# Optimization experiments

Measured on AMD Instinct MI355X. Metric: run time of the kernel, lower is better.

The kernel has to match this reference:

```python
import jax, jax.numpy as jnp
import numpy as np
from jax import lax

# Config (matches init_kwargs): TrajGRU per HKO-7 reference impl (Shi et al.)
B, T, Cin, H, W = 8, 12, 1, 128, 128
F_, L = 64, 5            # out_channels (hidden filters), num trajectories
h_, w_ = H // 2, W // 2  # post-downsample spatial size


def _conv(x, w, b, stride=1, pad=0):
    y = lax.conv_general_dilated(x, w, (stride, stride), [(pad, pad), (pad, pad)],
                                 dimension_numbers=('NCHW', 'OIHW', 'NCHW'))
    return y + b[None, :, None, None]


def _leaky(x):
    return jnp.where(x >= 0, x, 0.2 * x)  # LeakyReLU(0.2)


def _warp_multi(img, flows):
    # img: (B,C,h,w); flows: (B,L,2,h,w) pixel displacements.
    # Bilinear grid_sample with zero padding; the HKO normalization
    # (2*v/(W-1)-1) followed by align_corners=True denormalization is the
    # identity, so we sample directly at grid + flow in pixel space.
    Bb, C, Hh, Ww = img.shape
    x = jnp.arange(Ww, dtype=img.dtype)[None, None, None, :] + flows[:, :, 0]  # (B,L,h,w)
    y = jnp.arange(Hh, dtype=img.dtype)[None, None, :, None] + flows[:, :, 1]
    x0 = jnp.floor(x); y0 = jnp.floor(y)
    x1 = x0 + 1.0;     y1 = y0 + 1.0
    imgl = img.transpose(0, 2, 3, 1)  # (B,h,w,C)
    bidx = jnp.arange(Bb)[:, None, None, None]

    def gather(xi, yi):
        valid = (xi >= 0) & (xi <= Ww - 1) & (yi >= 0) & (yi <= Hh - 1)
        xic = jnp.clip(xi, 0, Ww - 1).astype(jnp.int32)
        yic = jnp.clip(yi, 0, Hh - 1).astype(jnp.int32)
        return imgl[bidx, yic, xic] * valid[..., None].astype(img.dtype)  # (B,L,h,w,C)

    wa = ((x1 - x) * (y1 - y))[..., None]
    wb = ((x1 - x) * (y - y0))[..., None]
    wc = ((x - x0) * (y1 - y))[..., None]
    wd = ((x - x0) * (y - y0))[..., None]
    out = wa * gather(x0, y0) + wb * gather(x0, y1) + wc * gather(x1, y0) + wd * gather(x1, y1)
    # concat L warped copies along channels: (B,L,h,w,C) -> (B, L*C, h, w)
    return out.transpose(0, 1, 4, 2, 3).reshape(Bb, L * C, Hh, Ww)


def setup_inputs() -> dict:
    key = jax.random.key(0)
    ks = jax.random.split(key, 13)
    def rn(k, shape, s=0.05):
        return jax.random.normal(k, shape, dtype=jnp.float32) * s
    return {
        'x': jax.random.normal(ks[0], (B, T, Cin, H, W), dtype=jnp.float32),
        'W_down': rn(ks[1], (F_ * T, Cin * T, 4, 4)),
        'b_down': rn(ks[2], (F_ * T,)),
        'W_i2h': rn(ks[3], (3 * F_, F_, 3, 3)),
        'b_i2h': rn(ks[4], (3 * F_,)),
        'W_i2f': rn(ks[5], (32, F_, 5, 5)),
        'b_i2f': rn(ks[6], (32,)),
        'W_h2f': rn(ks[7], (32, F_, 5, 5)),
        'b_h2f': rn(ks[8], (32,)),
        'W_flow': rn(ks[9], (2 * L, 32, 5, 5), 0.02),
        'b_flow': rn(ks[10], (2 * L,), 0.02),
        'W_ret': rn(ks[11], (3 * F_, L * F_, 1, 1)),
        'b_ret': rn(ks[12], (3 * F_,)),
    }


def reference(x, W_down, b_down, W_i2h, b_i2h, W_i2f, b_i2f, W_h2f, b_h2f,
              W_flow, b_flow, W_ret, b_ret):
    Bb = x.shape[0]
    # downsample conv (k=4,s=2,p=1) + LeakyReLU(0.2) on time-stacked channels
    xd = _leaky(_conv(x.reshape(Bb, T * Cin, H, W), W_down, b_down, stride=2, pad=1))
    seq = xd.reshape(Bb, T, F_, h_, w_).transpose(1, 0, 2, 3, 4)  # (T,B,F,h,w)

    # input-dependent convs are batched across all timesteps up front
    flat = seq.reshape(T * Bb, F_, h_, w_)
    i2h_all = _conv(flat, W_i2h, b_i2h, pad=1).reshape(T, Bb, 3 * F_, h_, w_)
    i2f_all = _conv(flat, W_i2f, b_i2f, pad=2).reshape(T, Bb, 32, h_, w_)

    def step(hprev, inp):
        i2h_t, i2f_t = inp
        # flow generator: leaky(i2f(x_t) + h2f(h)) -> flows conv -> L 2-ch flows
        f1 = _leaky(i2f_t + _conv(hprev, W_h2f, b_h2f, pad=2))
        flows = _conv(f1, W_flow, b_flow, pad=2).reshape(Bb, L, 2, h_, w_)
        warped = _warp_multi(hprev, -flows)          # (B, L*F, h, w)
        h2h = _conv(warped, W_ret, b_ret)            # 1x1 projection -> (B, 3F, h, w)
        ir, iu, im = jnp.split(i2h_t, 3, axis=1)
        hr, hu, hm = jnp.split(h2h, 3, axis=1)
        r = jax.nn.sigmoid(ir + hr)
        u = jax.nn.sigmoid(iu + hu)
        m = _leaky(im + r * hm)
        hnew = u * hprev + (1.0 - u) * m
        return hnew, hnew

    h0 = jnp.zeros((Bb, F_, h_, w_), x.dtype)
    _, outs = lax.scan(step, h0, (i2h_all, i2f_all))  # (T,B,F,h,w)
    return outs.transpose(1, 0, 2, 3, 4)              # (B,T,F,h,w)
```

## Files before the change

### kernel.cpp

```cpp
#include <hip/hip_runtime.h>
#include <cstdint>

typedef long long ll;
typedef __bf16 bf16x8 __attribute__((ext_vector_type(8)));
typedef float f32x4 __attribute__((ext_vector_type(4)));
typedef unsigned int u32x4 __attribute__((ext_vector_type(4)));

#define NB 8
#define NT 12
#define NF 64
#define HWSZ 4096
#define I2H_T ((ll)NB * 4096 * 192)
#define I2F_T ((ll)NB * 4096 * 32)

struct alignas(8)  bh4 { __bf16 h[4]; };
struct alignas(16) bh8 { __bf16 h[8]; };

static __device__ inline f32x4 mfma16(bf16x8 a, bf16x8 b, f32x4 c) {
  return __builtin_amdgcn_mfma_f32_16x16x32_bf16(a, b, c, 0, 0, 0);
}
static __device__ inline bf16x8 ld8(const __bf16* p) {
  u32x4 u = *(const u32x4*)p;
  return __builtin_bit_cast(bf16x8, u);
}
static __device__ inline void st4(__bf16* p, float a0, float a1, float a2, float a3) {
  bh4 t; t.h[0] = (__bf16)a0; t.h[1] = (__bf16)a1; t.h[2] = (__bf16)a2; t.h[3] = (__bf16)a3;
  *(bh4*)p = t;
}
static __device__ inline float lky(float a) { return a >= 0.f ? a : 0.2f * a; }

static __device__ inline int swz_bid() {
  int bid = blockIdx.x;
  return ((gridDim.x & 7) == 0) ? (bid & 7) * (gridDim.x >> 3) + (bid >> 3) : bid;
}

static __device__ inline void step_decode(int& b, int& y, int& xh) {
  int bid = blockIdx.x;
  int oct = bid & 7, s = bid >> 3;
  b = s >> 4;
  int r = s & 15;
  y = oct * 8 + (r >> 1);
  xh = r & 1;
}

template<int W, int HALO>
static __device__ void stage8(__bf16* dst, const __bf16* grow) {
  int tid = threadIdx.x;
  u32x4 zz = {0u, 0u, 0u, 0u};
  #pragma unroll
  for (int it = 0; it < 2; ++it) {
    int i = tid + it * 256;
    int xr = i >> 3, g = i & 7, xi = xr + HALO;
    u32x4 v = zz;
    if (grow) v = *(const u32x4*)(grow + xr * 64 + g * 8);
    *(u32x4*)(dst + (g * W + xi) * 8) = v;
  }
  if (tid < 16 * HALO) {
    int h = tid >> 3, g = tid & 7;
    int xi = (h < HALO) ? h : 64 + h;
    *(u32x4*)(dst + (g * W + xi) * 8) = zz;
  }
}

__global__ __launch_bounds__(256) void k_prep(
    const float* __restrict__ Wd, const float* __restrict__ Wc,
    const float* __restrict__ Wi, const float* __restrict__ Wh,
    const float* __restrict__ Wfl, const float* __restrict__ Wret,
    __bf16* __restrict__ Adown, __bf16* __restrict__ Ai2h,
    __bf16* __restrict__ Afi, __bf16* __restrict__ Afh,
    __bf16* __restrict__ Afl, __bf16* __restrict__ Aret) {
  int n = blockIdx.x * 256 + threadIdx.x;
  if (n < 147456) {
    Adown[n] = (__bf16)Wd[n];
  } else if (n < 258048) {
    int i = n - 147456;
    int tap = i / 12288, o = (i % 12288) / 64, c = i % 64;
    Ai2h[i] = (__bf16)Wc[(o * 64 + c) * 9 + tap];
  } else if (n < 309248) {
    int i = n - 258048;
    int tap = i / 2048, o = (i % 2048) / 64, c = i % 64;
    Afi[i] = (__bf16)Wi[(o * 64 + c) * 25 + tap];
  } else if (n < 360448) {
    int i = n - 309248;
    int tap = i / 2048, o = (i % 2048) / 64, c = i % 64;
    Afh[i] = (__bf16)Wh[(o * 64 + c) * 25 + tap];
  } else if (n < 373248) {
    int i = n - 360448;
    int tap = i / 512, o = (i % 512) / 32, c = i % 32;
    Afl[i] = (__bf16)(o < 10 ? Wfl[(o * 32 + c) * 25 + tap] : 0.f);
  } else if (n < 434688) {
    Aret[n - 373248] = (__bf16)Wret[n - 373248];
  }
}

__global__ __launch_bounds__(256) void k_down(
    const float* __restrict__ x, const __bf16* __restrict__ Adown,
    const float* __restrict__ bd, __bf16* __restrict__ seq) {
  __shared__ __bf16 smd[6240];
  int bi = swz_bid();
  int zQ = bi & 3, y = (bi >> 2) & 63, b = bi >> 8;
  int tid = threadIdx.x;
  for (int i = tid; i < 6240; i += 256) {
    int ic = i / 520, rem = i % 520, ky = rem / 130, xi = rem % 130;
    int ix = xi - 1, iy = 2 * y - 1 + ky;
    float v = (ix >= 0 && ix < 128 && iy >= 0 && iy < 128)
                  ? x[(((ll)(b * 12 + ic) * 128 + iy) << 7) + ix] : 0.f;
    smd[i] = (__bf16)v;
  }
  __syncthreads();
  int wv = __builtin_amdgcn_readfirstlane(tid >> 6);
  int lane = tid & 63, q = lane >> 4, lr = lane & 15;
  int px = wv * 16 + lr;
  f32x4 zv = {0.f, 0.f, 0.f, 0.f};
  f32x4 acc[12];
  #pragma unroll
  for (int mt = 0; mt < 12; ++mt) acc[mt] = zv;

  for (int ks = 0; ks < 6; ++ks) {
    int k0 = ks * 32 + q * 8;
    int ic = k0 >> 4, ky0 = (k0 >> 2) & 3;
    const __bf16* rp = smd + (ic * 4 + ky0) * 130 + 2 * px;
    bh8 bb;
    #pragma unroll
    for (int j = 0; j < 8; ++j)
      bb.h[j] = rp[(j >> 2) * 130 + (j & 3)];
    bf16x8 bfr = __builtin_bit_cast(bf16x8, bb);
    #pragma unroll
    for (int mt = 0; mt < 12; ++mt) {
      bf16x8 afr = ld8(Adown + ((ll)(zQ * 192 + mt * 16 + lr) * 192 + k0));
      acc[mt] = mfma16(afr, bfr, acc[mt]);
    }
  }
  #pragma unroll
  for (int mt = 0; mt < 12; ++mt) {
    int t_idx = zQ * 3 + (mt >> 2);
    int f0 = (mt & 3) * 16 + q * 4;
    float v[4];
    #pragma unroll
    for (int r = 0; r < 4; ++r)
      v[r] = lky(acc[mt][r] + bd[zQ * 192 + mt * 16 + q * 4 + r]);
    st4(seq + (((ll)(t_idx * NB + b) * 4096 + y * 64 + px) * 64 + f0),
        v[0], v[1], v[2], v[3]);
  }
}

__global__ __launch_bounds__(256, 2) void k_i2h4(
    const __bf16* __restrict__ in0, const __bf16* __restrict__ A,
    const float* __restrict__ bc, __bf16* __restrict__ out0) {
  __shared__ __align__(16) __bf16 smI[6 * 8 * 67 * 8];
  __shared__ __align__(16) __bf16 smA[2][96 * 64];
  int bi_ = swz_bid();
  int yg = bi_ & 15, och = (bi_ >> 4) & 1, tb = bi_ >> 5;
  int y0 = yg * 4;
  const __bf16* base = in0 + (ll)tb * (4096 * 64);
  const __bf16* Ab = A + ((ll)och * 96) * 64;
  int tid = threadIdx.x;
  u32x4 ar[3];
  auto loadA = [&](int tap) {
    #pragma unroll
    for (int it = 0; it < 3; ++it) {
      int j = it * 256 + tid;
      ar[it] = *(const u32x4*)(Ab + (ll)tap * (192 * 64) + j * 8);
    }
  };
  auto writeA = [&](int buf) {
    #pragma unroll
    for (int it = 0; it < 3; ++it) {
      int j = it * 256 + tid;
      int oc = j >> 3, g = j & 7;
      *(u32x4*)(smA[buf] + oc * 64 + ((g ^ (oc & 7)) * 8)) = ar[it];
    }
  };
  loadA(0);
  #pragma unroll
  for (int s = 0; s < 6; ++s) {
    int yr = y0 - 1 + s;
    stage8<67, 1>(smI + s * (8 * 67 * 8),
                  (yr >= 0 && yr < 64) ? base + (ll)yr * 64 * 64 : nullptr);
  }
  writeA(0);
  __syncthreads();

  int wv = __builtin_amdgcn_readfirstlane(tid >> 6);
  int lane = tid & 63, q = lane >> 4, lr = lane & 15;
  int mh = wv & 1, rg = wv >> 1;
  f32x4 zv = {0.f, 0.f, 0.f, 0.f};
  f32x4 acc[3][8];
  #pragma unroll
  for (int mt = 0; mt < 3; ++mt)
    #pragma unroll
    for (int nt = 0; nt < 8; ++nt) acc[mt][nt] = zv;

  for (int tap = 0; tap < 9; ++tap) {
    if (tap < 8) loadA(tap + 1);
    int ky = tap / 3, kx = tap % 3;
    const __bf16* Ax = smA[tap & 1];
    #pragma unroll
    for (int ks = 0; ks < 2; ++ks) {
      bf16x8 afr[3];
      #pragma unroll
      for (int mt = 0; mt < 3; ++mt) {
        int oc = mh * 48 + mt * 16 + lr;
        afr[mt] = ld8(Ax + oc * 64 + (((ks * 4 + q) ^ (lr & 7)) * 8));
      }
      bf16x8 bfr[8];
      #pragma unroll
      for (int rl = 0; rl < 2; ++rl)
        #pragma unroll
        for (int nx = 0; nx < 4; ++nx) {
          int s = rg * 2 + rl + ky;
          bfr[rl * 4 + nx] =
              ld8(smI + ((s * 8 + ks * 4 + q) * 67 + nx * 16 + lr + kx) * 8);
        }
      #pragma unroll
      for (int mt = 0; mt < 3; ++mt)
        #pragma unroll
        for (int nt = 0; nt < 8; ++nt)
          acc[mt][nt] = mfma16(afr[mt], bfr[nt], acc[mt][nt]);
    }
    if (tap < 8) writeA((tap + 1) & 1);
    __syncthreads();
  }

  #pragma unroll
  for (int rl = 0; rl < 2; ++rl)
    #pragma unroll
    for (int nx = 0; nx < 4; ++nx) {
      int row = y0 + rg * 2 + rl, px = nx * 16 + lr;
      __bf16* op = out0 + ((ll)tb * 4096 + row * 64 + px) * 192;
      #pragma unroll
      for (int mt = 0; mt < 3; ++mt) {
        int oc0 = och * 96 + mh * 48 + mt * 16 + q * 4;
        f32x4 a = acc[mt][rl * 4 + nx];
        st4(op + oc0, a[0] + bc[oc0], a[1] + bc[oc0 + 1],
                      a[2] + bc[oc0 + 2], a[3] + bc[oc0 + 3]);
      }
    }
}

__global__ __launch_bounds__(256, 2) void k_i2fb(
    const __bf16* __restrict__ in0, const __bf16* __restrict__ A,
    __bf16* __restrict__ out0) {
  __shared__ __align__(16) __bf16 smI[8 * 8 * 69 * 8];
  __shared__ __align__(16) __bf16 smA[2][32 * 64];
  float* red = (float*)smI;
  int bi_ = swz_bid();
  int yg = bi_ & 15, tb = bi_ >> 4;
  int y0 = yg * 4;
  const __bf16* base = in0 + (ll)tb * (4096 * 64);
  int tid = threadIdx.x;
  u32x4 ar;
  auto loadA = [&](int tap) { ar = *(const u32x4*)(A + (ll)tap * 2048 + tid * 8); };
  auto writeA = [&](int buf) {
    int oc = tid >> 3, g = tid & 7;
    *(u32x4*)(smA[buf] + oc * 64 + ((g ^ (oc & 7)) * 8)) = ar;
  };
  loadA(0);
  #pragma unroll
  for (int s = 0; s < 8; ++s) {
    int yr = y0 - 2 + s;
    stage8<69, 2>(smI + s * (8 * 69 * 8),
                  (yr >= 0 && yr < 64) ? base + (ll)yr * 64 * 64 : nullptr);
  }
  writeA(0);
  __syncthreads();

  int wv = __builtin_amdgcn_readfirstlane(tid >> 6);
  int lane = tid & 63, q = lane >> 4, lr = lane & 15;
  int rg = wv & 1, ksh = wv >> 1;
  f32x4 zv = {0.f, 0.f, 0.f, 0.f};
  f32x4 acc[2][8];
  #pragma unroll
  for (int mt = 0; mt < 2; ++mt)
    #pragma unroll
    for (int nt = 0; nt < 8; ++nt) acc[mt][nt] = zv;

  for (int tap = 0; tap < 25; ++tap) {
    if (tap < 24) loadA(tap + 1);
    int ky = tap / 5, kx = tap % 5;
    const __bf16* Ax = smA[tap & 1];
    bf16x8 afr[2];
    #pragma unroll
    for (int mt = 0; mt < 2; ++mt) {
      int oc = mt * 16 + lr;
      afr[mt] = ld8(Ax + oc * 64 + (((ksh * 4 + q) ^ (lr & 7)) * 8));
    }
    bf16x8 bfr[8];
    #pragma unroll
    for (int rl = 0; rl < 2; ++rl)
      #pragma unroll
      for (int nx = 0; nx < 4; ++nx) {
        int s = rg * 2 + rl + ky;
        bfr[rl * 4 + nx] =
            ld8(smI + ((s * 8 + ksh * 4 + q) * 69 + nx * 16 + lr + kx) * 8);
      }
    #pragma unroll
    for (int mt = 0; mt < 2; ++mt)
      #pragma unroll
      for (int nt = 0; nt < 8; ++nt)
        acc[mt][nt] = mfma16(afr[mt], bfr[nt], acc[mt][nt]);
    if (tap < 24) writeA((tap + 1) & 1);
    __syncthreads();
  }

  if (ksh == 1) {
    #pragma unroll
    for (int mt = 0; mt < 2; ++mt)
      #pragma unroll
      for (int rl = 0; rl < 2; ++rl)
        #pragma unroll
        for (int nx = 0; nx < 4; ++nx) {
          int row_l = rg * 2 + rl, px = nx * 16 + lr;
          int oc = mt * 16 + q * 4;
          f32x4 a = acc[mt][rl * 4 + nx];
          #pragma unroll
          for (int r = 0; r < 4; ++r)
            red[(row_l * 64 + px) * 33 + oc + r] = a[r];
        }
  }
  __syncthreads();
  if (ksh == 0) {
    #pragma unroll
    for (int mt = 0; mt < 2; ++mt)
      #pragma unroll
      for (int rl = 0; rl < 2; ++rl)
        #pragma unroll
        for (int nx = 0; nx < 4; ++nx) {
          int row_l = rg * 2 + rl, px = nx * 16 + lr;
          int oc0 = mt * 16 + q * 4;
          f32x4 a = acc[mt][rl * 4 + nx];
          float v[4];
          #pragma unroll
          for (int r = 0; r < 4; ++r)
            v[r] = a[r] + red[(row_l * 64 + px) * 33 + oc0 + r];
          st4(out0 + ((ll)tb * 4096 + (y0 + row_l) * 64 + px) * 32 + oc0,
              v[0], v[1], v[2], v[3]);
        }
  }
}

#define STEP_SMEM_BYTES (25344 + 2176)

static __device__ void dev_h2f(char* smraw, int t0,
    const __bf16* __restrict__ hb, const __bf16* __restrict__ A,
    const float* __restrict__ bi, const float* __restrict__ bh,
    const __bf16* __restrict__ i2f_t, __bf16* __restrict__ f1buf,
    int b, int y, int xh) {
  __bf16* smI = (__bf16*)smraw;
  float* red = (float*)smraw;
  int x0 = xh * 32;
  int tid = threadIdx.x;
  int wv = __builtin_amdgcn_readfirstlane(tid >> 6);
  int lane = tid & 63, q = lane >> 4, lr = lane & 15;

  int pxl_e = tid >> 3, oc0_e = (tid & 7) * 4;
  bh4 iv = *(const bh4*)(i2f_t + ((ll)(b * 64 + y) * 64 + x0 + pxl_e) * 32 + oc0_e);

  bf16x8 cur[2][2], nxt[2][2];
  auto loadAt = [&](int tap, bf16x8 a[2][2]) {
    #pragma unroll
    for (int ks = 0; ks < 2; ++ks)
      #pragma unroll
      for (int mt = 0; mt < 2; ++mt)
        a[ks][mt] = ld8(A + ((ll)(tap * 32 + mt * 16 + lr) * 64 + ks * 32 + q * 8));
  };
  loadAt(wv, cur);

  u32x4 zz = {0u, 0u, 0u, 0u};
  for (int i = tid; i < 5 * 296; i += 256) {
    int s = i / 296, rem = i % 296, xi = rem >> 3, g = rem & 7;
    int yr = y - 2 + s, xg = x0 - 2 + xi;
    u32x4 v = zz;
    if (!t0 && yr >= 0 && yr < 64 && xg >= 0 && xg < 64)
      v = *(const u32x4*)(hb + ((ll)(b * 64 + yr) * 64 + xg) * 64 + g * 8);
    *(u32x4*)(smI + ((s * 8 + g) * 37 + xi) * 8) = v;
  }
  __syncthreads();

  f32x4 zv = {0.f, 0.f, 0.f, 0.f};
  f32x4 acc[2][2];
  #pragma unroll
  for (int mt = 0; mt < 2; ++mt)
    #pragma unroll
    for (int nx = 0; nx < 2; ++nx) acc[mt][nx] = zv;

  #pragma unroll
  for (int j = 0; j < 7; ++j) {
    int tap = 4 * j + wv;
    if (tap < 25) {
      if (tap + 4 < 25) loadAt(tap + 4, nxt);
      int ky = tap / 5, kx = tap % 5;
      #pragma unroll
      for (int ks = 0; ks < 2; ++ks) {
        bf16x8 bfr[2];
        #pragma unroll
        for (int nx = 0; nx < 2; ++nx)
          bfr[nx] = ld8(smI + ((ky * 8 + ks * 4 + q) * 37 + nx * 16 + lr + kx) * 8);
        #pragma unroll
        for (int mt = 0; mt < 2; ++mt)
          #pragma unroll
          for (int nx = 0; nx < 2; ++nx)
            acc[mt][nx] = mfma16(cur[ks][mt], bfr[nx], acc[mt][nx]);
      }
      #pragma unroll
      for (int ks = 0; ks < 2; ++ks)
        #pragma unroll
        for (int mt = 0; mt < 2; ++mt) cur[ks][mt] = nxt[ks][mt];
    }
  }
  __syncthreads();

  #pragma unroll
  for (int mt = 0; mt < 2; ++mt)
    #pragma unroll
    for (int nx = 0; nx < 2; ++nx) {
      int pxl = nx * 16 + lr, oc = mt * 16 + q * 4;
      f32x4 a = acc[mt][nx];
      #pragma unroll
      for (int r = 0; r < 4; ++r)
        red[wv * 1056 + pxl * 33 + oc + r] = a[r];
    }
  __syncthreads();

  float v[4];
  #pragma unroll
  for (int r = 0; r < 4; ++r) {
    float s = red[0 * 1056 + pxl_e * 33 + oc0_e + r] + red[1 * 1056 + pxl_e * 33 + oc0_e + r] +
              red[2 * 1056 + pxl_e * 33 + oc0_e + r] + red[3 * 1056 + pxl_e * 33 + oc0_e + r];
    v[r] = lky(s + (float)iv.h[r] + bi[oc0_e + r] + bh[oc0_e + r]);
  }
  st4(f1buf + ((ll)(b * 64 + y) * 64 + x0 + pxl_e) * 32 + oc0_e, v[0], v[1], v[2], v[3]);
}

static __device__ void dev_fwr(char* smraw, int t0,
    const __bf16* __restrict__ f1buf, const __bf16* __restrict__ Afl,
    const float* __restrict__ bfl, const __bf16* __restrict__ hb,
    const __bf16* __restrict__ Aret, const float* __restrict__ br,
    const __bf16* __restrict__ i2h_t, const float* __restrict__ hprevf,
    float* __restrict__ outp, ll osb, __bf16* __restrict__ hbc,
    int b, int y, int xh) {
  float* exbuf = (float*)smraw;
  float* flows = (float*)(smraw + 25344);
  __bf16* f1l = (__bf16*)smraw;
  __bf16* wrp = (__bf16*)smraw;
  int x0 = xh * 32;
  int tid = threadIdx.x;
  int wv = __builtin_amdgcn_readfirstlane(tid >> 6);
  int lane = tid & 63, q = lane >> 4, lr = lane & 15;

  int pxl_e = tid >> 3, f0_e = (tid & 7) * 8;
  int xg_e = x0 + pxl_e;
  const __bf16* ih = i2h_t + ((ll)(b * 64 + y) * 64 + xg_e) * 192;
  bh8 irv = *(const bh8*)(ih + f0_e);
  bh8 iuv = *(const bh8*)(ih + 64 + f0_e);
  bh8 imv = *(const bh8*)(ih + 128 + f0_e);
  float h0j[8];
  const float* hp = hprevf + (ll)b * osb + y * 64 + xg_e;
  #pragma unroll
  for (int j = 0; j < 8; ++j)
    h0j[j] = t0 ? 0.f : hp[(ll)(f0_e + j) << 12];

  u32x4 zz = {0u, 0u, 0u, 0u};
  for (int i = tid; i < 5 * 148; i += 256) {
    int s = i / 148, rem = i % 148, xi = rem >> 2, g = rem & 3;
    int yr = y - 2 + s, xg = x0 - 2 + xi;
    u32x4 v = zz;
    if (yr >= 0 && yr < 64 && xg >= 0 && xg < 64)
      v = *(const u32x4*)(f1buf + ((ll)(b * 64 + yr) * 64 + xg) * 32 + g * 8);
    *(u32x4*)(f1l + ((s * 4 + g) * 37 + xi) * 8) = v;
  }
  __syncthreads();

  if (wv < 2) {
    f32x4 acc1 = {0.f, 0.f, 0.f, 0.f};
    #pragma unroll
    for (int tap = 0; tap < 25; ++tap) {
      int ky = tap / 5, kx = tap % 5;
      bf16x8 bfr = ld8(f1l + ((ky * 4 + q) * 37 + wv * 16 + lr + kx) * 8);
      bf16x8 afr = ld8(Afl + ((ll)(tap * 16 + lr) * 32 + q * 8));
      acc1 = mfma16(afr, bfr, acc1);
    }
    #pragma unroll
    for (int r = 0; r < 4; ++r) {
      int oc = q * 4 + r;
      flows[(wv * 16 + lr) * 17 + oc] = acc1[r] + (oc < 10 ? bfl[oc] : 0.f);
    }
  }
  __syncthreads();

  {
    int pxl = tid & 31, cg = tid >> 5;
    int xw = x0 + pxl;
    const __bf16* hbb = hb + ((ll)b << 18);
    #pragma unroll
    for (int l = 0; l < 5; ++l) {
      bh8 ov;
      if (t0) {
        #pragma unroll
        for (int i = 0; i < 8; ++i) ov.h[i] = (__bf16)0.f;
      } else {
        float fx = flows[pxl * 17 + 2 * l];
        float fy = flows[pxl * 17 + 2 * l + 1];
        float pxf = (float)xw - fx, pyf = (float)y - fy;
        float x0f = floorf(pxf), y0f = floorf(pyf);
        int xx0 = (int)x0f, yy0 = (int)y0f, xx1 = xx0 + 1, yy1 = yy0 + 1;
        float dx = pxf - x0f, dy = pyf - y0f;
        bool vx0 = xx0 >= 0 && xx0 <= 63, vx1 = xx1 >= 0 && xx1 <= 63;
        bool vy0 = yy0 >= 0 && yy0 <= 63, vy1 = yy1 >= 0 && yy1 <= 63;
        float wA = (vx0 && vy0) ? (1.f - dx) * (1.f - dy) : 0.f;
        float wB = (vx0 && vy1) ? (1.f - dx) * dy : 0.f;
        float wC = (vx1 && vy0) ? dx * (1.f - dy) : 0.f;
        float wD = (vx1 && vy1) ? dx * dy : 0.f;
        int cx0 = min(max(xx0, 0), 63), cx1 = min(max(xx1, 0), 63);
        int cy0 = min(max(yy0, 0), 63), cy1 = min(max(yy1, 0), 63);
        int o00 = (cy0 * 64 + cx0) * 64, o10 = (cy1 * 64 + cx0) * 64;
        int o01 = (cy0 * 64 + cx1) * 64, o11 = (cy1 * 64 + cx1) * 64;
        int c0 = cg * 8;
        bf16x8 aA = ld8(hbb + o00 + c0), aB = ld8(hbb + o10 + c0);
        bf16x8 aC = ld8(hbb + o01 + c0), aD = ld8(hbb + o11 + c0);
        #pragma unroll
        for (int i = 0; i < 8; ++i)
          ov.h[i] = (__bf16)(wA * (float)aA[i] + wB * (float)aB[i] +
                             wC * (float)aC[i] + wD * (float)aD[i]);
      }
      int G = l * 8 + cg;
      int Gs = (G & ~7) | ((G & 7) ^ ((tid & 31) & 7));
      *(bh8*)(wrp + ((tid & 31) * 40 + Gs) * 8) = ov;
    }
  }
  __syncthreads();

  f32x4 zv = {0.f, 0.f, 0.f, 0.f};
  f32x4 acc[3][2];
  #pragma unroll
  for (int mt = 0; mt < 3; ++mt)
    #pragma unroll
    for (int nt = 0; nt < 2; ++nt) acc[mt][nt] = zv;
  bf16x8 cA[3], nA[3];
  auto loadAr = [&](int ks, bf16x8* a) {
    #pragma unroll
    for (int mt = 0; mt < 3; ++mt)
      a[mt] = ld8(Aret + ((ll)((wv * 3 + mt) * 16 + lr) * 320 + ks * 32 + q * 8));
  };
  loadAr(0, cA);
  #pragma unroll
  for (int ks = 0; ks < 10; ++ks) {
    if (ks < 9) loadAr(ks + 1, nA);
    bf16x8 bfr[2];
    #pragma unroll
    for (int nt = 0; nt < 2; ++nt) {
      int pxl = nt * 16 + lr;
      int Gr = ks * 4 + q;
      int Gs = (Gr & ~7) | ((Gr & 7) ^ (pxl & 7));
      bfr[nt] = ld8(wrp + (pxl * 40 + Gs) * 8);
    }
    #pragma unroll
    for (int mt = 0; mt < 3; ++mt)
      #pragma unroll
      for (int nt = 0; nt < 2; ++nt)
        acc[mt][nt] = mfma16(cA[mt], bfr[nt], acc[mt][nt]);
    #pragma unroll
    for (int mt = 0; mt < 3; ++mt) cA[mt] = nA[mt];
  }
  __syncthreads();

  #pragma unroll
  for (int mt = 0; mt < 3; ++mt)
    #pragma unroll
    for (int nt = 0; nt < 2; ++nt) {
      int oc = (wv * 3 + mt) * 16 + q * 4;
      int pxl = nt * 16 + lr;
      #pragma unroll
      for (int r = 0; r < 4; ++r)
        exbuf[(oc + r) * 33 + pxl] = acc[mt][nt][r];
    }
  __syncthreads();

  float* ob = outp + (ll)b * osb + y * 64 + xg_e;
  __bf16* hc = hbc + ((ll)(b * 64 + y) * 64 + xg_e) * 64 + f0_e;
  bh8 hv;
  #pragma unroll
  for (int j = 0; j < 8; ++j) {
    int f = f0_e + j;
    float hr = exbuf[f * 33 + pxl_e] + br[f];
    float hu = exbuf[(f + 64) * 33 + pxl_e] + br[f + 64];
    float hm = exbuf[(f + 128) * 33 + pxl_e] + br[f + 128];
    float rr = 1.f / (1.f + __expf(-((float)irv.h[j] + hr)));
    float uu = 1.f / (1.f + __expf(-((float)iuv.h[j] + hu)));
    float m = lky((float)imv.h[j] + rr * hm);
    float hn = uu * h0j[j] + (1.f - uu) * m;
    ob[(ll)f << 12] = hn;
    hv.h[j] = (__bf16)hn;
  }
  *(bh8*)hc = hv;
}

__global__ __launch_bounds__(256, 4) void k_h2f5(
    int t0, const __bf16* hb, const __bf16* A, const float* bi, const float* bh,
    const __bf16* i2f_t, __bf16* f1buf) {
  __shared__ __align__(16) char smraw[STEP_SMEM_BYTES];
  int b, y, xh;
  step_decode(b, y, xh);
  dev_h2f(smraw, t0, hb, A, bi, bh, i2f_t, f1buf, b, y, xh);
}

__global__ __launch_bounds__(256, 4) void k_fwr2(
    int t0, const __bf16* f1buf, const __bf16* Afl, const float* bfl,
    const __bf16* hb, const __bf16* Aret, const float* br,
    const __bf16* i2h_t, const float* hprevf,
    float* outp, ll osb, __bf16* hbc) {
  __shared__ __align__(16) char smraw[STEP_SMEM_BYTES];
  int b, y, xh;
  step_decode(b, y, xh);
  dev_fwr(smraw, t0, f1buf, Afl, bfl, hb, Aret, br, i2h_t, hprevf,
          outp, osb, hbc, b, y, xh);
}

extern "C" void kernel_launch(void* const* d_in, const int* in_sizes, int n_in,
                              void* d_out, int out_size, void* d_ws, size_t ws_size,
                              hipStream_t stream) {
  const float* x      = (const float*)d_in[0];
  const float* W_down = (const float*)d_in[1];
  const float* b_down = (const float*)d_in[2];
  const float* W_i2h  = (const float*)d_in[3];
  const float* b_i2h  = (const float*)d_in[4];
  const float* W_i2f  = (const float*)d_in[5];
  const float* b_i2f  = (const float*)d_in[6];
  const float* W_h2f  = (const float*)d_in[7];
  const float* b_h2f  = (const float*)d_in[8];
  const float* W_flow = (const float*)d_in[9];
  const float* b_flow = (const float*)d_in[10];
  const float* W_ret  = (const float*)d_in[11];
  const float* b_ret  = (const float*)d_in[12];
  float* out = (float*)d_out;

  const ll H_N = (ll)NB * 4096 * 64;

  auto align256 = [](ll v) { return (v + 255) & ~255LL; };
  ll fixed = 0;
  fixed += align256(147456LL * 2);
  fixed += align256(110592LL * 2);
  fixed += align256(51200LL * 2) * 2;
  fixed += align256(12800LL * 2);
  fixed += align256(61440LL * 2);
  fixed += align256((ll)NT * NB * 4096 * 64 * 2);
  fixed += align256((ll)NB * 4096 * 32 * 2);
  fixed += align256(H_N * 2) * 2;
  ll need_full = fixed + align256(NT * I2H_T * 2) + align256(NT * I2F_T * 2);
  int fits = (need_full <= (ll)ws_size);
  int slabT = fits ? NT : 1;

  char* p = (char*)d_ws;
  auto alloc = [&](ll bytes) { char* r = p; p += (bytes + 255) & ~255LL; return r; };
  __bf16* Adown  = (__bf16*)alloc(147456LL * 2);
  __bf16* Ai2h   = (__bf16*)alloc(110592LL * 2);
  __bf16* Afi    = (__bf16*)alloc(51200LL * 2);
  __bf16* Afh    = (__bf16*)alloc(51200LL * 2);
  __bf16* Afl    = (__bf16*)alloc(12800LL * 2);
  __bf16* Aret   = (__bf16*)alloc(61440LL * 2);
  __bf16* seq    = (__bf16*)alloc((ll)NT * NB * 4096 * 64 * 2);
  __bf16* f1buf  = (__bf16*)alloc((ll)NB * 4096 * 32 * 2);
  __bf16* hbufA  = (__bf16*)alloc(H_N * 2);
  __bf16* hbufB  = (__bf16*)alloc(H_N * 2);
  __bf16* i2h_sl = (__bf16*)alloc(slabT * I2H_T * 2);
  __bf16* i2f_sl = (__bf16*)alloc(slabT * I2F_T * 2);
  if (p > (char*)d_ws + ws_size) return;

  k_prep<<<1698, 256, 0, stream>>>(W_down, W_i2h, W_i2f, W_h2f, W_flow, W_ret,
                                   Adown, Ai2h, Afi, Afh, Afl, Aret);
  k_down<<<NB * 64 * 4, 256, 0, stream>>>(x, Adown, b_down, seq);

  if (fits) {
    k_i2h4<<<NT * NB * 2 * 16, 256, 0, stream>>>(seq, Ai2h, b_i2h, i2h_sl);
    k_i2fb<<<NT * NB * 16, 256, 0, stream>>>(seq, Afi, i2f_sl);
  }

  const ll osb = (ll)NT * NF * HWSZ;
  for (int t = 0; t < NT; ++t) {
    const __bf16* xt0 = seq + (ll)t * NB * 4096 * 64;
    if (!fits) {
      k_i2h4<<<NB * 2 * 16, 256, 0, stream>>>(xt0, Ai2h, b_i2h, i2h_sl);
      k_i2fb<<<NB * 16, 256, 0, stream>>>(xt0, Afi, i2f_sl);
    }
    int ti = fits ? t : 0;
    const __bf16* hb = (t & 1) ? hbufA : hbufB;
    __bf16* hbc = (t & 1) ? hbufB : hbufA;
    const float* hpf = (t == 0) ? out : out + (ll)(t - 1) * NF * HWSZ;

    k_h2f5<<<NB * 64 * 2, 256, 0, stream>>>((t == 0) ? 1 : 0, hb, Afh,
                                            b_i2f, b_h2f,
                                            i2f_sl + (ll)ti * I2F_T, f1buf);
    k_fwr2<<<NB * 64 * 2, 256, 0, stream>>>((t == 0) ? 1 : 0, f1buf, Afl,
                                            b_flow, hb, Aret, b_ret,
                                            i2h_sl + (ll)ti * I2H_T, hpf,
                                            out + (ll)t * NF * HWSZ, osb, hbc);
  }
}
```

Baseline: 837.8 us.

## Preload all conv weight taps into LDS and retile i2h/i2f convolutions

The batched i2h (3x3) and i2f (5x5) convolution kernels now stage every weight tap into shared memory once, instead of double-buffering one tap at a time with a barrier per tap. Each block covers a smaller tile: i2h takes 48 output channels by 4 rows, and i2f takes 2 rows with the K dimension split into two halves. The i2f kernel loses its cross-wave reduction through shared memory, and the grid grows to give more blocks. In exchange there is more redundant input staging, larger LDS use that allows only one block per CU, and fewer MFMAs per wave to hide latency.

```diff
diff --git a/kernel.cpp b/kernel.cpp
--- a/kernel.cpp
+++ b/kernel.cpp
@@ -57,6 +57,23 @@
   }
   if (tid < 16 * HALO) {
     int h = tid >> 3, g = tid & 7;
+    int xi = (h < HALO) ? h : 64 + h;
+    *(u32x4*)(dst + (g * W + xi) * 8) = zz;
+  }
+}
+
+template<int W, int HALO>
+static __device__ void stage_half(__bf16* dst, const __bf16* grow, int goff) {
+  int tid = threadIdx.x;
+  u32x4 zz = {0u, 0u, 0u, 0u};
+  {
+    int xr = tid >> 2, g = tid & 3, xi = xr + HALO;
+    u32x4 v = zz;
+    if (grow) v = *(const u32x4*)(grow + xr * 64 + (goff + g) * 8);
+    *(u32x4*)(dst + (g * W + xi) * 8) = v;
+  }
+  if (tid < 8 * HALO) {
+    int h = tid >> 2, g = tid & 3;
     int xi = (h < HALO) ? h : 64 + h;
     *(u32x4*)(dst + (g * W + xi) * 8) = zz;
   }
@@ -144,198 +161,154 @@
   }
 }
 
-__global__ __launch_bounds__(256, 2) void k_i2h4(
+__global__ __launch_bounds__(256, 1) void k_i2h5(
     const __bf16* __restrict__ in0, const __bf16* __restrict__ A,
     const float* __restrict__ bc, __bf16* __restrict__ out0) {
-  __shared__ __align__(16) __bf16 smI[6 * 8 * 67 * 8];
-  __shared__ __align__(16) __bf16 smA[2][96 * 64];
+  __shared__ __align__(16) __bf16 smA[9 * 48 * 64];
+  __shared__ __align__(16) __bf16 smI[6 * 8 * 66 * 8];
   int bi_ = swz_bid();
-  int yg = bi_ & 15, och = (bi_ >> 4) & 1, tb = bi_ >> 5;
-  int y0 = yg * 4;
-  const __bf16* base = in0 + (ll)tb * (4096 * 64);
-  const __bf16* Ab = A + ((ll)och * 96) * 64;
-  int tid = threadIdx.x;
-  u32x4 ar[3];
-  auto loadA = [&](int tap) {
-    #pragma unroll
-    for (int it = 0; it < 3; ++it) {
-      int j = it * 256 + tid;
-      ar[it] = *(const u32x4*)(Ab + (ll)tap * (192 * 64) + j * 8);
-    }
-  };
-  auto writeA = [&](int buf) {
-    #pragma unroll
-    for (int it = 0; it < 3; ++it) {
-      int j = it * 256 + tid;
-      int oc = j >> 3, g = j & 7;
-      *(u32x4*)(smA[buf] + oc * 64 + ((g ^ (oc & 7)) * 8)) = ar[it];
-    }
-  };
-  loadA(0);
-  #pragma unroll
-  for (int s = 0; s < 6; ++s) {
-    int yr = y0 - 1 + s;
-    stage8<67, 1>(smI + s * (8 * 67 * 8),
-                  (yr >= 0 && yr < 64) ? base + (ll)yr * 64 * 64 : nullptr);
-  }
-  writeA(0);
-  __syncthreads();
-
-  int wv = __builtin_amdgcn_readfirstlane(tid >> 6);
-  int lane = tid & 63, q = lane >> 4, lr = lane & 15;
-  int mh = wv & 1, rg = wv >> 1;
-  f32x4 zv = {0.f, 0.f, 0.f, 0.f};
-  f32x4 acc[3][8];
-  #pragma unroll
-  for (int mt = 0; mt < 3; ++mt)
-    #pragma unroll
-    for (int nt = 0; nt < 8; ++nt) acc[mt][nt] = zv;
-
-  for (int tap = 0; tap < 9; ++tap) {
-    if (tap < 8) loadA(tap + 1);
-    int ky = tap / 3, kx = tap % 3;
-    const __bf16* Ax = smA[tap & 1];
-    #pragma unroll
-    for (int ks = 0; ks < 2; ++ks) {
-      bf16x8 afr[3];
-      #pragma unroll
-      for (int mt = 0; mt < 3; ++mt) {
-        int oc = mh * 48 + mt * 16 + lr;
-        afr[mt] = ld8(Ax + oc * 64 + (((ks * 4 + q) ^ (lr & 7)) * 8));
-      }
-      bf16x8 bfr[8];
-      #pragma unroll
-      for (int rl = 0; rl < 2; ++rl)
-        #pragma unroll
-        for (int nx = 0; nx < 4; ++nx) {
-          int s = rg * 2 + rl + ky;
-          bfr[rl * 4 + nx] =
-              ld8(smI + ((s * 8 + ks * 4 + q) * 67 + nx * 16 + lr + kx) * 8);
-        }
-      #pragma unroll
-      for (int mt = 0; mt < 3; ++mt)
-        #pragma unroll
-        for (int nt = 0; nt < 8; ++nt)
-          acc[mt][nt] = mfma16(afr[mt], bfr[nt], acc[mt][nt]);
-    }
-    if (tap < 8) writeA((tap + 1) & 1);
-    __syncthreads();
-  }
-
-  #pragma unroll
-  for (int rl = 0; rl < 2; ++rl)
-    #pragma unroll
-    for (int nx = 0; nx < 4; ++nx) {
-      int row = y0 + rg * 2 + rl, px = nx * 16 + lr;
-      __bf16* op = out0 + ((ll)tb * 4096 + row * 64 + px) * 192;
-      #pragma unroll
-      for (int mt = 0; mt < 3; ++mt) {
-        int oc0 = och * 96 + mh * 48 + mt * 16 + q * 4;
-        f32x4 a = acc[mt][rl * 4 + nx];
-        st4(op + oc0, a[0] + bc[oc0], a[1] + bc[oc0 + 1],
-                      a[2] + bc[oc0 + 2], a[3] + bc[oc0 + 3]);
-      }
-    }
-}
-
-__global__ __launch_bounds__(256, 2) void k_i2fb(
-    const __bf16* __restrict__ in0, const __bf16* __restrict__ A,
-    __bf16* __restrict__ out0) {
-  __shared__ __align__(16) __bf16 smI[8 * 8 * 69 * 8];
-  __shared__ __align__(16) __bf16 smA[2][32 * 64];
-  float* red = (float*)smI;
-  int bi_ = swz_bid();
-  int yg = bi_ & 15, tb = bi_ >> 4;
+  int yg = bi_ & 15, oq = (bi_ >> 4) & 3, tb = bi_ >> 6;
   int y0 = yg * 4;
   const __bf16* base = in0 + (ll)tb * (4096 * 64);
   int tid = threadIdx.x;
-  u32x4 ar;
-  auto loadA = [&](int tap) { ar = *(const u32x4*)(A + (ll)tap * 2048 + tid * 8); };
-  auto writeA = [&](int buf) {
-    int oc = tid >> 3, g = tid & 7;
-    *(u32x4*)(smA[buf] + oc * 64 + ((g ^ (oc & 7)) * 8)) = ar;
-  };
-  loadA(0);
-  #pragma unroll
-  for (int s = 0; s < 8; ++s) {
-    int yr = y0 - 2 + s;
-    stage8<69, 2>(smI + s * (8 * 69 * 8),
+
+  for (int j = tid; j < 6912; j += 256) {
+    int tap = j / 384, r = j % 384, ocl = r >> 3, g = r & 7;
+    u32x4 v = *(const u32x4*)(A + (ll)tap * (192 * 64) + (oq * 48 + ocl) * 64 + g * 8);
+    *(u32x4*)(smA + ((ll)(tap * 48 + ocl)) * 64 + ((g ^ (ocl & 7)) * 8)) = v;
+  }
+  #pragma unroll
+  for (int s = 0; s < 6; ++s) {
+    int yr = y0 - 1 + s;
+    stage8<66, 1>(smI + s * (8 * 66 * 8),
                   (yr >= 0 && yr < 64) ? base + (ll)yr * 64 * 64 : nullptr);
   }
-  writeA(0);
   __syncthreads();
 
   int wv = __builtin_amdgcn_readfirstlane(tid >> 6);
   int lane = tid & 63, q = lane >> 4, lr = lane & 15;
-  int rg = wv & 1, ksh = wv >> 1;
+  int rg = wv;
   f32x4 zv = {0.f, 0.f, 0.f, 0.f};
-  f32x4 acc[2][8];
+  f32x4 acc[3][4];
+  #pragma unroll
+  for (int mt = 0; mt < 3; ++mt)
+    #pragma unroll
+    for (int nt = 0; nt < 4; ++nt) acc[mt][nt] = zv;
+
+  #pragma unroll
+  for (int tap = 0; tap < 9; ++tap) {
+    int ky = tap / 3, kx = tap % 3;
+    #pragma unroll
+    for (int ks = 0; ks < 2; ++ks) {
+      bf16x8 afr[3];
+      #pragma unroll
+      for (int mt = 0; mt < 3; ++mt) {
+        int ocl = mt * 16 + lr;
+        afr[mt] = ld8(smA + ((ll)(tap * 48 + ocl)) * 64 +
+                      (((ks * 4 + q) ^ (ocl & 7)) * 8));
+      }
+      bf16x8 bfr[4];
+      #pragma unroll
+      for (int nt = 0; nt < 4; ++nt) {
+        int s = rg + ky;
+        bfr[nt] = ld8(smI + ((s * 8 + ks * 4 + q) * 66 + nt * 16 + lr + kx) * 8);
+      }
+      #pragma unroll
+      for (int mt = 0; mt < 3; ++mt)
+        #pragma unroll
+        for (int nt = 0; nt < 4; ++nt)
+          acc[mt][nt] = mfma16(afr[mt], bfr[nt], acc[mt][nt]);
+    }
+  }
+
+  int row = y0 + rg;
+  #pragma unroll
+  for (int nt = 0; nt < 4; ++nt) {
+    int px = nt * 16 + lr;
+    __bf16* op = out0 + ((ll)tb * 4096 + row * 64 + px) * 192;
+    #pragma unroll
+    for (int mt = 0; mt < 3; ++mt) {
+      int oc0 = oq * 48 + mt * 16 + q * 4;
+      f32x4 a = acc[mt][nt];
+      st4(op + oc0, a[0] + bc[oc0], a[1] + bc[oc0 + 1],
+                    a[2] + bc[oc0 + 2], a[3] + bc[oc0 + 3]);
+    }
+  }
+}
+
+__global__ __launch_bounds__(256, 1) void k_i2fb2(
+    const __bf16* __restrict__ in0, const __bf16* __restrict__ A,
+    __bf16* __restrict__ out0) {
+  __shared__ __align__(16) __bf16 smA[25 * 32 * 64];
+  __shared__ __align__(16) __bf16 smI[6 * 4 * 69 * 8];
+  int bi_ = swz_bid();
+  int yg = bi_ & 31, tb = bi_ >> 5;
+  int y0 = yg * 2;
+  const __bf16* base = in0 + (ll)tb * (4096 * 64);
+  int tid = threadIdx.x;
+
+  for (int j = tid; j < 6400; j += 256) {
+    int tap = j >> 8, r = j & 255, oc = r >> 3, g = r & 7;
+    u32x4 v = *(const u32x4*)(A + (ll)tap * 2048 + oc * 64 + g * 8);
+    *(u32x4*)(smA + ((ll)(tap * 32 + oc)) * 64 + ((g ^ (oc & 7)) * 8)) = v;
+  }
+
+  int wv = __builtin_amdgcn_readfirstlane(tid >> 6);
+  int lane = tid & 63, q = lane >> 4, lr = lane & 15;
+  int rg = wv & 1, xh = wv >> 1;
+  f32x4 zv = {0.f, 0.f, 0.f, 0.f};
+  f32x4 acc[2][2];
   #pragma unroll
   for (int mt = 0; mt < 2; ++mt)
     #pragma unroll
-    for (int nt = 0; nt < 8; ++nt) acc[mt][nt] = zv;
-
-  for (int tap = 0; tap < 25; ++tap) {
-    if (tap < 24) loadA(tap + 1);
-    int ky = tap / 5, kx = tap % 5;
-    const __bf16* Ax = smA[tap & 1];
-    bf16x8 afr[2];
+    for (int nt = 0; nt < 2; ++nt) acc[mt][nt] = zv;
+
+  #pragma unroll
+  for (int ks = 0; ks < 2; ++ks) {
+    if (ks) __syncthreads();
+    #pragma unroll
+    for (int s = 0; s < 6; ++s) {
+      int yr = y0 - 2 + s;
+      stage_half<69, 2>(smI + s * (4 * 69 * 8),
+                        (yr >= 0 && yr < 64) ? base + (ll)yr * 64 * 64 : nullptr,
+                        ks * 4);
+    }
+    __syncthreads();
+    #pragma unroll
+    for (int tap = 0; tap < 25; ++tap) {
+      int ky = tap / 5, kx = tap % 5;
+      bf16x8 afr[2];
+      #pragma unroll
+      for (int mt = 0; mt < 2; ++mt) {
+        int oc = mt * 16 + lr;
+        afr[mt] = ld8(smA + ((ll)(tap * 32 + oc)) * 64 +
+                      (((ks * 4 + q) ^ (oc & 7)) * 8));
+      }
+      bf16x8 bfr[2];
+      #pragma unroll
+      for (int nt = 0; nt < 2; ++nt) {
+        int s = rg + ky;
+        bfr[nt] = ld8(smI + ((s * 4 + q) * 69 + xh * 32 + nt * 16 + lr + kx) * 8);
+      }
+      #pragma unroll
+      for (int mt = 0; mt < 2; ++mt)
+        #pragma unroll
+        for (int nt = 0; nt < 2; ++nt)
+          acc[mt][nt] = mfma16(afr[mt], bfr[nt], acc[mt][nt]);
+    }
+  }
+
+  int row = y0 + rg;
+  #pragma unroll
+  for (int nt = 0; nt < 2; ++nt) {
+    int px = xh * 32 + nt * 16 + lr;
+    __bf16* op = out0 + ((ll)tb * 4096 + row * 64 + px) * 32;
     #pragma unroll
     for (int mt = 0; mt < 2; ++mt) {
-      int oc = mt * 16 + lr;
-      afr[mt] = ld8(Ax + oc * 64 + (((ksh * 4 + q) ^ (lr & 7)) * 8));
-    }
-    bf16x8 bfr[8];
-    #pragma unroll
-    for (int rl = 0; rl < 2; ++rl)
-      #pragma unroll
-      for (int nx = 0; nx < 4; ++nx) {
-        int s = rg * 2 + rl + ky;
-        bfr[rl * 4 + nx] =
-            ld8(smI + ((s * 8 + ksh * 4 + q) * 69 + nx * 16 + lr + kx) * 8);
-      }
-    #pragma unroll
-    for (int mt = 0; mt < 2; ++mt)
-      #pragma unroll
-      for (int nt = 0; nt < 8; ++nt)
-        acc[mt][nt] = mfma16(afr[mt], bfr[nt], acc[mt][nt]);
-    if (tap < 24) writeA((tap + 1) & 1);
-    __syncthreads();
-  }
-
-  if (ksh == 1) {
-    #pragma unroll
-    for (int mt = 0; mt < 2; ++mt)
-      #pragma unroll
-      for (int rl = 0; rl < 2; ++rl)
-        #pragma unroll
-        for (int nx = 0; nx < 4; ++nx) {
-          int row_l = rg * 2 + rl, px = nx * 16 + lr;
-          int oc = mt * 16 + q * 4;
-          f32x4 a = acc[mt][rl * 4 + nx];
-          #pragma unroll
-          for (int r = 0; r < 4; ++r)
-            red[(row_l * 64 + px) * 33 + oc + r] = a[r];
-        }
-  }
-  __syncthreads();
-  if (ksh == 0) {
-    #pragma unroll
-    for (int mt = 0; mt < 2; ++mt)
-      #pragma unroll
-      for (int rl = 0; rl < 2; ++rl)
-        #pragma unroll
-        for (int nx = 0; nx < 4; ++nx) {
-          int row_l = rg * 2 + rl, px = nx * 16 + lr;
-          int oc0 = mt * 16 + q * 4;
-          f32x4 a = acc[mt][rl * 4 + nx];
-          float v[4];
-          #pragma unroll
-          for (int r = 0; r < 4; ++r)
-            v[r] = a[r] + red[(row_l * 64 + px) * 33 + oc0 + r];
-          st4(out0 + ((ll)tb * 4096 + (y0 + row_l) * 64 + px) * 32 + oc0,
-              v[0], v[1], v[2], v[3]);
-        }
+      int oc0 = mt * 16 + q * 4;
+      f32x4 a = acc[mt][nt];
+      st4(op + oc0, a[0], a[1], a[2], a[3]);
+    }
   }
 }
 
@@ -671,16 +644,16 @@
   k_down<<<NB * 64 * 4, 256, 0, stream>>>(x, Adown, b_down, seq);
 
   if (fits) {
-    k_i2h4<<<NT * NB * 2 * 16, 256, 0, stream>>>(seq, Ai2h, b_i2h, i2h_sl);
-    k_i2fb<<<NT * NB * 16, 256, 0, stream>>>(seq, Afi, i2f_sl);
+    k_i2h5<<<NT * NB * 4 * 16, 256, 0, stream>>>(seq, Ai2h, b_i2h, i2h_sl);
+    k_i2fb2<<<NT * NB * 32, 256, 0, stream>>>(seq, Afi, i2f_sl);
   }
 
   const ll osb = (ll)NT * NF * HWSZ;
   for (int t = 0; t < NT; ++t) {
     const __bf16* xt0 = seq + (ll)t * NB * 4096 * 64;
     if (!fits) {
-      k_i2h4<<<NB * 2 * 16, 256, 0, stream>>>(xt0, Ai2h, b_i2h, i2h_sl);
-      k_i2fb<<<NB * 16, 256, 0, stream>>>(xt0, Afi, i2f_sl);
+      k_i2h5<<<NB * 4 * 16, 256, 0, stream>>>(xt0, Ai2h, b_i2h, i2h_sl);
+      k_i2fb2<<<NB * 32, 256, 0, stream>>>(xt0, Afi, i2f_sl);
     }
     int ti = fits ? t : 0;
     const __bf16* hb = (t & 1) ? hbufA : hbufB;
```

New measurement: 1.032 ms. +23.1%, slower.
